# Kernel optimization log

Measured on AMD Instinct MI355X. Metric: run time of the kernel, lower is better.

The kernel has to match this reference:

```python
import jax, jax.numpy as jnp
import numpy as np

S = 1024          # num tokens (single prefill sequence)
H = 2880          # hidden_size
NH = 64           # num query heads
NKV = 8           # num kv heads
HD = 64           # head_dim
G = NH // NKV     # query heads per kv head
THETA = 10000.0
SCALE = HD ** -0.5


def _rope(x, positions):
    # neox-style rotary over full head_dim; x: [S, n_heads, HD]
    half = HD // 2
    inv_freq = 1.0 / (THETA ** (jnp.arange(half, dtype=jnp.float32) / half))
    ang = positions.astype(jnp.float32)[:, None] * inv_freq          # [S, half]
    cos = jnp.cos(ang)[:, None, :]
    sin = jnp.sin(ang)[:, None, :]
    x1, x2 = x[..., :half], x[..., half:]
    return jnp.concatenate([x1 * cos - x2 * sin, x2 * cos + x1 * sin], axis=-1)


def setup_inputs() -> dict:
    key = jax.random.key(0)
    k0, k1, k2, k3 = jax.random.split(key, 4)
    return {
        "positions": jnp.arange(S, dtype=jnp.int32),
        "hidden_states": jax.random.normal(k0, (S, H), dtype=jnp.float32),
        "qkv_w": jax.random.normal(k1, ((NH + 2 * NKV) * HD, H), dtype=jnp.float32) * 0.02,
        "o_w": jax.random.normal(k2, (H, NH * HD), dtype=jnp.float32) * 0.02,
        "sinks": jax.random.normal(k3, (NH,), dtype=jnp.float32),
    }


def reference(positions, hidden_states, qkv_w, o_w, sinks):
    # fused QKV projection (no bias, matching attention_bias=False)
    qkv = hidden_states @ qkv_w.T                                     # [S, 5120]
    q = qkv[:, : NH * HD].reshape(S, NH, HD)
    k = qkv[:, NH * HD : NH * HD + NKV * HD].reshape(S, NKV, HD)
    v = qkv[:, NH * HD + NKV * HD :].reshape(S, NKV, HD)

    # rotary on q and k (rotary_dim == head_dim)
    q = _rope(q, positions)
    k = _rope(k, positions)

    # GQA: group query heads by kv head -> [S, NKV, G, HD]
    qg = q.reshape(S, NKV, G, HD)

    logits = jnp.einsum("qghd,kgd->ghqk", qg, k) * SCALE              # [NKV, G, S, S]
    causal = positions[:, None] >= positions[None, :]                 # [S, S]
    logits = jnp.where(causal[None, None], logits, -jnp.inf)

    # attention sinks: per-head extra logit in the softmax denominator,
    # contributing no value vector.
    sink = sinks.reshape(NKV, G)[:, :, None, None]                    # [NKV, G, 1, 1]
    m = jnp.maximum(jnp.max(logits, axis=-1, keepdims=True), sink)
    p = jnp.exp(logits - m)                                           # [NKV, G, S, S]
    denom = jnp.sum(p, axis=-1, keepdims=True) + jnp.exp(sink - m)
    attn = jnp.einsum("ghqk,kgd->qghd", p / denom, v)                 # [S, NKV, G, HD]

    out = attn.reshape(S, NH * HD) @ o_w.T                            # [S, H]
    return out
```

## Files before the change

### kernel.cpp

```cpp
#include <hip/hip_runtime.h>
#include <hip/hip_bf16.h>
#include <math.h>

#define S_LEN 1024
#define HDIM  2880
#define NH    64
#define NKV   8
#define HD    64
#define QKV_N ((NH + 2*NKV) * HD)
#define O_K   (NH * HD)
#define SCALE 0.125f

typedef _Float16 f16x8 __attribute__((ext_vector_type(8)));
typedef _Float16 f16x4 __attribute__((ext_vector_type(4)));
typedef float    f32x4 __attribute__((ext_vector_type(4)));

__global__ __launch_bounds__(256) void cvt_f32_f16(const float* __restrict__ src,
                                                   _Float16* __restrict__ dst, int n4) {
    const int stride = gridDim.x * blockDim.x;
    for (int i = blockIdx.x * blockDim.x + threadIdx.x; i < n4; i += stride) {
        const float4 v = ((const float4*)src)[i];
        f16x4 p;
        p[0] = (_Float16)v.x; p[1] = (_Float16)v.y;
        p[2] = (_Float16)v.z; p[3] = (_Float16)v.w;
        ((f16x4*)dst)[i] = p;
    }
}

#define CSTR 68
template<typename CT>
__global__ __launch_bounds__(256) void gemm_f16(const _Float16* __restrict__ A,
                                                const float* __restrict__ B,
                                                CT* __restrict__ C,
                                                int M, int N, int K) {
    __shared__ __align__(16) _Float16 sh[16384];

    const int tid  = threadIdx.x;
    const int lane = tid & 63;
    const int wave = tid >> 6;
    const int wr   = wave >> 1;
    const int wc   = wave & 1;
    const int quad = lane >> 4;
    const int fr   = lane & 15;
    const int ks   = quad * 8;
    const int row0 = blockIdx.y * 128;
    const int col0 = blockIdx.x * 128;

    const int klen   = K / (int)gridDim.z;
    const int kb     = (int)blockIdx.z * klen;
    const int nsteps = klen / 32;
    CT* Cp = C + (size_t)blockIdx.z * M * N;

    const int a_cbase0 = wave * 64;
    const int a_ci0 = a_cbase0 + lane;
    const int a_r0 = a_ci0 >> 2, a_ch0 = a_ci0 & 3;
    const int a_cbase1 = 256 + wave * 64;
    const int a_ci1 = a_cbase1 + lane;
    const int a_r1 = a_ci1 >> 2, a_ch1 = a_ci1 & 3;
    int b_r[4], b_ch[4];
#pragma unroll
    for (int it = 0; it < 4; ++it) {
        const int c4 = it * 256 + tid;
        b_r[it]  = c4 >> 3;
        b_ch[it] = (c4 & 7) << 2;
    }

    float4 breg[4];
    f32x4 acc[4][4] = {};

    {
        const _Float16* gp0 = A + (size_t)(row0 + a_r0) * K + kb + a_ch0 * 8;
        __builtin_amdgcn_global_load_lds(
            (const __attribute__((address_space(1))) void*)gp0,
            (__attribute__((address_space(3))) void*)(sh + (size_t)a_cbase0 * 8), 16, 0, 0);
        const _Float16* gp1 = A + (size_t)(row0 + a_r1) * K + kb + a_ch1 * 8;
        __builtin_amdgcn_global_load_lds(
            (const __attribute__((address_space(1))) void*)gp1,
            (__attribute__((address_space(3))) void*)(sh + (size_t)a_cbase1 * 8), 16, 0, 0);
#pragma unroll
        for (int it = 0; it < 4; ++it) {
            int brow = col0 + b_r[it];
            if (brow >= N) brow = N - 1;
            breg[it] = *(const float4*)&B[(size_t)brow * K + kb + b_ch[it]];
        }
        _Float16* Bs0 = sh + 8192;
#pragma unroll
        for (int it = 0; it < 4; ++it) {
            f16x4 p;
            p[0] = (_Float16)breg[it].x; p[1] = (_Float16)breg[it].y;
            p[2] = (_Float16)breg[it].z; p[3] = (_Float16)breg[it].w;
            *(f16x4*)&Bs0[b_r[it] * 32 + b_ch[it]] = p;
        }
    }

    for (int step = 0; step < nsteps; ++step) {
        const int cur = step & 1;
        const int nxt = cur ^ 1;
        _Float16* Acur = sh + cur * 4096;
        _Float16* Anxt = sh + nxt * 4096;
        _Float16* Bcur = sh + 8192 + cur * 4096;
        _Float16* Bnxt = sh + 8192 + nxt * 4096;

        __syncthreads();

        const bool more = (step + 1 < nsteps);
        if (more) {
            const int k1 = kb + (step + 1) * 32;
            const _Float16* gp0 = A + (size_t)(row0 + a_r0) * K + k1 + a_ch0 * 8;
            __builtin_amdgcn_global_load_lds(
                (const __attribute__((address_space(1))) void*)gp0,
                (__attribute__((address_space(3))) void*)(Anxt + (size_t)a_cbase0 * 8), 16, 0, 0);
            const _Float16* gp1 = A + (size_t)(row0 + a_r1) * K + k1 + a_ch1 * 8;
            __builtin_amdgcn_global_load_lds(
                (const __attribute__((address_space(1))) void*)gp1,
                (__attribute__((address_space(3))) void*)(Anxt + (size_t)a_cbase1 * 8), 16, 0, 0);
#pragma unroll
            for (int it = 0; it < 4; ++it) {
                int brow = col0 + b_r[it];
                if (brow >= N) brow = N - 1;
                breg[it] = *(const float4*)&B[(size_t)brow * K + k1 + b_ch[it]];
            }
        }

        f16x8 af[4], bfr[4];
#pragma unroll
        for (int mi = 0; mi < 4; ++mi)
            af[mi] = *(const f16x8*)&Acur[(wr * 64 + mi * 16 + fr) * 32 + ks];
#pragma unroll
        for (int ni = 0; ni < 4; ++ni)
            bfr[ni] = *(const f16x8*)&Bcur[(wc * 64 + ni * 16 + fr) * 32 + ks];
#pragma unroll
        for (int mi = 0; mi < 4; ++mi)
#pragma unroll
            for (int ni = 0; ni < 4; ++ni)
                acc[mi][ni] = __builtin_amdgcn_mfma_f32_16x16x32_f16(
                    af[mi], bfr[ni], acc[mi][ni], 0, 0, 0);

        if (more) {
#pragma unroll
            for (int it = 0; it < 4; ++it) {
                f16x4 p;
                p[0] = (_Float16)breg[it].x; p[1] = (_Float16)breg[it].y;
                p[2] = (_Float16)breg[it].z; p[3] = (_Float16)breg[it].w;
                *(f16x4*)&Bnxt[b_r[it] * 32 + b_ch[it]] = p;
            }
        }
    }

#pragma unroll
    for (int p = 0; p < 2; ++p) {
        __syncthreads();
        if (wc == p) {
#pragma unroll
            for (int mi = 0; mi < 4; ++mi)
#pragma unroll
                for (int ni = 0; ni < 4; ++ni) {
                    const f32x4 v = acc[mi][ni];
#pragma unroll
                    for (int r = 0; r < 4; ++r)
                        sh[(wr * 64 + mi * 16 + quad * 4 + r) * CSTR + ni * 16 + fr] =
                            (_Float16)v[r];
                }
        }
        __syncthreads();
#pragma unroll
        for (int it = 0; it < 4; ++it) {
            const int id  = it * 256 + tid;
            const int row = id >> 3;
            const int ch  = (id & 7) * 8;
            const int col = col0 + p * 64 + ch;
            if (col < N) {
                const f16x4 lo = *(const f16x4*)&sh[row * CSTR + ch];
                const f16x4 hi = *(const f16x4*)&sh[row * CSTR + ch + 4];
                if constexpr (sizeof(CT) == 2) {
                    f16x8 v;
                    v[0]=lo[0]; v[1]=lo[1]; v[2]=lo[2]; v[3]=lo[3];
                    v[4]=hi[0]; v[5]=hi[1]; v[6]=hi[2]; v[7]=hi[3];
                    *(f16x8*)&Cp[(size_t)(row0 + row) * N + col] = v;
                } else {
                    float4 v0 = make_float4((float)lo[0], (float)lo[1],
                                            (float)lo[2], (float)lo[3]);
                    float4 v1 = make_float4((float)hi[0], (float)hi[1],
                                            (float)hi[2], (float)hi[3]);
                    *(float4*)&Cp[(size_t)(row0 + row) * N + col]     = v0;
                    *(float4*)&Cp[(size_t)(row0 + row) * N + col + 4] = v1;
                }
            }
        }
    }
}

__global__ __launch_bounds__(256) void rope_reduce(_Float16* __restrict__ parts,
                                                   int nsplit,
                                                   _Float16* __restrict__ vt,
                                                   const int* __restrict__ positions) {
    __shared__ float buf[QKV_N];
    const int s   = blockIdx.x;
    const int tid = threadIdx.x;
    const size_t PSTR = (size_t)S_LEN * QKV_N;

    for (int c = tid; c < QKV_N / 4; c += 256) {
        float4 a = make_float4(0.f, 0.f, 0.f, 0.f);
        for (int j = 0; j < nsplit; ++j) {
            const f16x4 v = ((const f16x4*)(parts + j * PSTR + (size_t)s * QKV_N))[c];
            a.x += (float)v[0]; a.y += (float)v[1];
            a.z += (float)v[2]; a.w += (float)v[3];
        }
        ((float4*)buf)[c] = a;
    }
    __syncthreads();

    const float pos = (float)positions[s];
    _Float16* orow = parts + (size_t)s * QKV_N;
    for (int w = tid; w < 72 * 32; w += 256) {
        const int h = w >> 5;
        const int t = w & 31;
        const float inv_freq = exp2f(-(float)t * (13.287712379549449f / 32.0f));
        const float ang = pos * inv_freq;
        float sn, cs;
        sincosf(ang, &sn, &cs);
        const float x1 = buf[h * 64 + t];
        const float x2 = buf[h * 64 + t + 32];
        orow[h * 64 + t]      = (_Float16)(x1 * cs - x2 * sn);
        orow[h * 64 + t + 32] = (_Float16)(x2 * cs + x1 * sn);
    }
    for (int c = tid; c < NKV * HD; c += 256)
        vt[(size_t)c * S_LEN + s] = (_Float16)buf[(NH + NKV) * HD + c];
}

__global__ __launch_bounds__(256) void o_reduce(const _Float16* __restrict__ parts,
                                                float* __restrict__ out,
                                                int n4, int nsplit) {
    const size_t PSTR = (size_t)S_LEN * HDIM;
    const int stride = gridDim.x * blockDim.x;
    for (int i = blockIdx.x * blockDim.x + threadIdx.x; i < n4; i += stride) {
        float4 a = make_float4(0.f, 0.f, 0.f, 0.f);
        for (int j = 0; j < nsplit; ++j) {
            const f16x4 v = ((const f16x4*)(parts + j * PSTR))[i];
            a.x += (float)v[0]; a.y += (float)v[1];
            a.z += (float)v[2]; a.w += (float)v[3];
        }
        ((float4*)out)[i] = a;
    }
}

#define LSTR 72
__global__ __launch_bounds__(256) void attn_mfma(const _Float16* __restrict__ qkv,
                                                 const _Float16* __restrict__ vt,
                                                 const float* __restrict__ sinks,
                                                 const int* __restrict__ positions,
                                                 _Float16* __restrict__ attn_out) {
    __shared__ __align__(16) _Float16 Ks[2][64 * LSTR];
    __shared__ __align__(16) _Float16 Vs[2][64 * LSTR];
    __shared__ __align__(16) _Float16 Ps[64 * LSTR];

    const int tid  = threadIdx.x;
    const int lane = tid & 63;
    const int wave = tid >> 6;
    const int fr   = lane & 15;
    const int quad = lane >> 4;
    const int ks8  = quad * 8;
    const int n    = blockIdx.x;
    const int qt   = (int)gridDim.y - 1 - (int)blockIdx.y;
    const int g    = n >> 3;

    int st_r[2], st_o[2];
#pragma unroll
    for (int it = 0; it < 2; ++it) {
        const int c = it * 256 + tid;
        st_r[it] = c >> 3;
        st_o[it] = (c & 7) * 8;
    }

    const _Float16* qrow = qkv + (size_t)(qt * 64 + wave * 16 + fr) * QKV_N + n * HD;
    const f16x8 a_q0 = *(const f16x8*)&qrow[ks8];
    const f16x8 a_q1 = *(const f16x8*)&qrow[32 + ks8];

    int pq[4];
#pragma unroll
    for (int r = 0; r < 4; ++r)
        pq[r] = positions[qt * 64 + wave * 16 + quad * 4 + r];

    const float sinkv = sinks[n];
    float m[4], l[4];
    f32x4 o[4] = {};
#pragma unroll
    for (int r = 0; r < 4; ++r) { m[r] = sinkv; l[r] = 1.0f; }

    f16x8 kreg[2], vreg[2];
    {
        const _Float16* Kg = qkv + (size_t)0 * QKV_N + NH * HD + g * HD;
        const _Float16* Vg = vt + (size_t)(g * HD) * S_LEN;
#pragma unroll
        for (int it = 0; it < 2; ++it) {
            kreg[it] = *(const f16x8*)&Kg[(size_t)st_r[it] * QKV_N + st_o[it]];
            vreg[it] = *(const f16x8*)&Vg[(size_t)st_r[it] * S_LEN + st_o[it]];
        }
#pragma unroll
        for (int it = 0; it < 2; ++it) {
            *(f16x8*)&Ks[0][st_r[it] * LSTR + st_o[it]] = kreg[it];
            *(f16x8*)&Vs[0][st_r[it] * LSTR + st_o[it]] = vreg[it];
        }
    }

    for (int kt = 0; kt <= qt; ++kt) {
        const int cur = kt & 1;
        const int nxt = cur ^ 1;
        __syncthreads();

        const bool more = (kt < qt);
        if (more) {
            const _Float16* Kg = qkv + (size_t)((kt + 1) * 64) * QKV_N + NH * HD + g * HD;
            const _Float16* Vg = vt + (size_t)(g * HD) * S_LEN + (kt + 1) * 64;
#pragma unroll
            for (int it = 0; it < 2; ++it) {
                kreg[it] = *(const f16x8*)&Kg[(size_t)st_r[it] * QKV_N + st_o[it]];
                vreg[it] = *(const f16x8*)&Vg[(size_t)st_r[it] * S_LEN + st_o[it]];
            }
        }

        f32x4 s[4] = {};
#pragma unroll
        for (int nt = 0; nt < 4; ++nt) {
            const f16x8 b0 = *(const f16x8*)&Ks[cur][(nt * 16 + fr) * LSTR + ks8];
            s[nt] = __builtin_amdgcn_mfma_f32_16x16x32_f16(a_q0, b0, s[nt], 0, 0, 0);
            const f16x8 b1 = *(const f16x8*)&Ks[cur][(nt * 16 + fr) * LSTR + 32 + ks8];
            s[nt] = __builtin_amdgcn_mfma_f32_16x16x32_f16(a_q1, b1, s[nt], 0, 0, 0);
        }

        const bool diag = (kt == qt);
        int pk[4];
        if (diag) {
#pragma unroll
            for (int nt = 0; nt < 4; ++nt) pk[nt] = positions[qt * 64 + nt * 16 + fr];
        }
#pragma unroll
        for (int nt = 0; nt < 4; ++nt)
#pragma unroll
            for (int r = 0; r < 4; ++r) {
                float sv = s[nt][r] * SCALE;
                if (diag && pk[nt] > pq[r]) sv = -3.0e38f;
                s[nt][r] = sv;
            }

#pragma unroll
        for (int r = 0; r < 4; ++r) {
            float tm = fmaxf(fmaxf(s[0][r], s[1][r]), fmaxf(s[2][r], s[3][r]));
            tm = fmaxf(tm, __shfl_xor(tm, 1, 64));
            tm = fmaxf(tm, __shfl_xor(tm, 2, 64));
            tm = fmaxf(tm, __shfl_xor(tm, 4, 64));
            tm = fmaxf(tm, __shfl_xor(tm, 8, 64));
            const float nm = fmaxf(m[r], tm);
            const float alpha = __expf(m[r] - nm);
            float rs = 0.0f;
#pragma unroll
            for (int nt = 0; nt < 4; ++nt) {
                const float p = __expf(s[nt][r] - nm);
                s[nt][r] = p;
                rs += p;
            }
            rs += __shfl_xor(rs, 1, 64);
            rs += __shfl_xor(rs, 2, 64);
            rs += __shfl_xor(rs, 4, 64);
            rs += __shfl_xor(rs, 8, 64);
            l[r] = l[r] * alpha + rs;
            m[r] = nm;
#pragma unroll
            for (int nt = 0; nt < 4; ++nt) o[nt][r] *= alpha;
        }

#pragma unroll
        for (int nt = 0; nt < 4; ++nt)
#pragma unroll
            for (int r = 0; r < 4; ++r)
                Ps[(wave * 16 + quad * 4 + r) * LSTR + nt * 16 + fr] = (_Float16)s[nt][r];
        __threadfence_block();

#pragma unroll
        for (int k2 = 0; k2 < 2; ++k2) {
            const f16x8 ap = *(const f16x8*)&Ps[(wave * 16 + fr) * LSTR + k2 * 32 + ks8];
#pragma unroll
            for (int nt = 0; nt < 4; ++nt) {
                const f16x8 bv = *(const f16x8*)&Vs[cur][(nt * 16 + fr) * LSTR + k2 * 32 + ks8];
                o[nt] = __builtin_amdgcn_mfma_f32_16x16x32_f16(ap, bv, o[nt], 0, 0, 0);
            }
        }

        if (more) {
#pragma unroll
            for (int it = 0; it < 2; ++it) {
                *(f16x8*)&Ks[nxt][st_r[it] * LSTR + st_o[it]] = kreg[it];
                *(f16x8*)&Vs[nxt][st_r[it] * LSTR + st_o[it]] = vreg[it];
            }
        }
    }

#pragma unroll
    for (int r = 0; r < 4; ++r) {
        const float inv = 1.0f / l[r];
        const size_t row = (size_t)(qt * 64 + wave * 16 + quad * 4 + r);
#pragma unroll
        for (int nt = 0; nt < 4; ++nt)
            attn_out[row * O_K + n * HD + nt * 16 + fr] = (_Float16)(o[nt][r] * inv);
    }
}

extern "C" void kernel_launch(void* const* d_in, const int* in_sizes, int n_in,
                              void* d_out, int out_size, void* d_ws, size_t ws_size,
                              hipStream_t stream) {
    const int*   positions = (const int*)d_in[0];
    const float* hidden    = (const float*)d_in[1];
    const float* qkv_w     = (const float*)d_in[2];
    const float* o_w       = (const float*)d_in[3];
    const float* sinks     = (const float*)d_in[4];
    float* out = (float*)d_out;

    const size_t n_hid  = (size_t)S_LEN * HDIM;
    const size_t n_qkv  = (size_t)S_LEN * QKV_N;
    const size_t n_attn = (size_t)S_LEN * O_K;
    const size_t n_vt   = (size_t)NKV * HD * S_LEN;
    const size_t n_out  = (size_t)S_LEN * HDIM;

    const int SP_Q = 3;
    const int SP_O = 4;

    const size_t need = (n_hid + SP_Q * n_qkv + n_attn + n_vt) * sizeof(_Float16);

    if (ws_size >= need) {
        _Float16* hid_h  = (_Float16*)d_ws;
        _Float16* qkvp   = hid_h + n_hid;
        _Float16* attn_h = qkvp + SP_Q * n_qkv;
        _Float16* vt     = attn_h + n_attn;
        _Float16* opart  = qkvp;

        cvt_f32_f16<<<512, 256, 0, stream>>>(hidden, hid_h, (int)(n_hid / 4));
        gemm_f16<_Float16><<<dim3(QKV_N / 128, S_LEN / 128, SP_Q), 256, 0, stream>>>(
            hid_h, qkv_w, qkvp, S_LEN, QKV_N, HDIM);
        rope_reduce<<<S_LEN, 256, 0, stream>>>(qkvp, SP_Q, vt, positions);
        attn_mfma<<<dim3(NH, S_LEN / 64), 256, 0, stream>>>(qkvp, vt, sinks, positions, attn_h);
        gemm_f16<_Float16><<<dim3((HDIM + 127) / 128, S_LEN / 128, SP_O), 256, 0, stream>>>(
            attn_h, o_w, opart, S_LEN, HDIM, O_K);
        o_reduce<<<1024, 256, 0, stream>>>(opart, out, (int)(n_out / 4), SP_O);
    } else {
        _Float16* hid_h  = (_Float16*)d_ws;
        _Float16* qkvp   = hid_h + n_hid;
        _Float16* attn_h = qkvp + n_qkv;
        _Float16* vt     = attn_h + n_attn;

        cvt_f32_f16<<<512, 256, 0, stream>>>(hidden, hid_h, (int)(n_hid / 4));
        gemm_f16<_Float16><<<dim3(QKV_N / 128, S_LEN / 128, 1), 256, 0, stream>>>(
            hid_h, qkv_w, qkvp, S_LEN, QKV_N, HDIM);
        rope_reduce<<<S_LEN, 256, 0, stream>>>(qkvp, 1, vt, positions);
        attn_mfma<<<dim3(NH, S_LEN / 64), 256, 0, stream>>>(qkvp, vt, sinks, positions, attn_h);
        gemm_f16<float><<<dim3((HDIM + 127) / 128, S_LEN / 128, 1), 256, 0, stream>>>(
            attn_h, o_w, out, S_LEN, HDIM, O_K);
    }
}
```

Measured before the change: 304.7 us.

## Pre-convert weights to fp16 and load both GEMM operands via direct LDS DMA

Adds a single conversion kernel that casts hidden states, QKV weights and output weights to fp16 in workspace. A new GEMM variant then loads both A and B tiles with global_load_lds DMA instead of register-staged fp32 loads followed by in-kernel conversion. The aim is to halve the GEMM's weight read traffic and drop the conversion and LDS store work from the inner loop. In exchange, every call pays an extra full read and fp16 write of both weight matrices, and it needs more workspace, with the old path kept as a fallback.

```diff
diff --git a/kernel.cpp b/kernel.cpp
--- a/kernel.cpp
+++ b/kernel.cpp
@@ -15,24 +15,46 @@
 typedef _Float16 f16x4 __attribute__((ext_vector_type(4)));
 typedef float    f32x4 __attribute__((ext_vector_type(4)));
 
+__device__ __forceinline__ void cvt4(const float* __restrict__ s,
+                                     _Float16* __restrict__ d, int i) {
+    const float4 v = ((const float4*)s)[i];
+    f16x4 p;
+    p[0] = (_Float16)v.x; p[1] = (_Float16)v.y;
+    p[2] = (_Float16)v.z; p[3] = (_Float16)v.w;
+    ((f16x4*)d)[i] = p;
+}
+
 __global__ __launch_bounds__(256) void cvt_f32_f16(const float* __restrict__ src,
                                                    _Float16* __restrict__ dst, int n4) {
     const int stride = gridDim.x * blockDim.x;
-    for (int i = blockIdx.x * blockDim.x + threadIdx.x; i < n4; i += stride) {
-        const float4 v = ((const float4*)src)[i];
-        f16x4 p;
-        p[0] = (_Float16)v.x; p[1] = (_Float16)v.y;
-        p[2] = (_Float16)v.z; p[3] = (_Float16)v.w;
-        ((f16x4*)dst)[i] = p;
-    }
+    for (int i = blockIdx.x * blockDim.x + threadIdx.x; i < n4; i += stride)
+        cvt4(src, dst, i);
+}
+
+__global__ __launch_bounds__(256) void cvt_all(const float* __restrict__ h,
+                                               const float* __restrict__ qw,
+                                               const float* __restrict__ ow,
+                                               _Float16* __restrict__ dh,
+                                               _Float16* __restrict__ dqw,
+                                               _Float16* __restrict__ dow) {
+    const int stride = gridDim.x * blockDim.x;
+    const int t0 = blockIdx.x * blockDim.x + threadIdx.x;
+    for (int i = t0; i < 737280;  i += stride) cvt4(h,  dh,  i);
+    for (int i = t0; i < 3686400; i += stride) cvt4(qw, dqw, i);
+    for (int i = t0; i < 2949120; i += stride) cvt4(ow, dow, i);
 }
 
 #define CSTR 68
+
+#define DMA16(GP, LP) __builtin_amdgcn_global_load_lds( \
+        (const __attribute__((address_space(1))) void*)(GP), \
+        (__attribute__((address_space(3))) void*)(LP), 16, 0, 0)
+
 template<typename CT>
-__global__ __launch_bounds__(256) void gemm_f16(const _Float16* __restrict__ A,
-                                                const float* __restrict__ B,
-                                                CT* __restrict__ C,
-                                                int M, int N, int K) {
+__global__ __launch_bounds__(256) void gemm_ff(const _Float16* __restrict__ A,
+                                               const _Float16* __restrict__ B,
+                                               CT* __restrict__ C,
+                                               int M, int N, int K) {
     __shared__ __align__(16) _Float16 sh[16384];
 
     const int tid  = threadIdx.x;
@@ -51,100 +73,57 @@
     const int nsteps = klen / 32;
     CT* Cp = C + (size_t)blockIdx.z * M * N;
 
-    const int a_cbase0 = wave * 64;
-    const int a_ci0 = a_cbase0 + lane;
-    const int a_r0 = a_ci0 >> 2, a_ch0 = a_ci0 & 3;
-    const int a_cbase1 = 256 + wave * 64;
-    const int a_ci1 = a_cbase1 + lane;
-    const int a_r1 = a_ci1 >> 2, a_ch1 = a_ci1 & 3;
-    int b_r[4], b_ch[4];
-#pragma unroll
-    for (int it = 0; it < 4; ++it) {
-        const int c4 = it * 256 + tid;
-        b_r[it]  = c4 >> 3;
-        b_ch[it] = (c4 & 7) << 2;
-    }
-
-    float4 breg[4];
+    const int r0   = tid >> 2;
+    const int ch   = (tid & 3) * 8;
+    const int dst0 = (tid & ~63) * 8;
+
+    const size_t aoff0 = (size_t)(row0 + r0)      * K;
+    const size_t aoff1 = (size_t)(row0 + r0 + 64) * K;
+    int bR0 = col0 + r0;      if (bR0 >= N) bR0 = N - 1;
+    int bR1 = col0 + r0 + 64; if (bR1 >= N) bR1 = N - 1;
+    const size_t boff0 = (size_t)bR0 * K;
+    const size_t boff1 = (size_t)bR1 * K;
+
     f32x4 acc[4][4] = {};
 
     {
-        const _Float16* gp0 = A + (size_t)(row0 + a_r0) * K + kb + a_ch0 * 8;
-        __builtin_amdgcn_global_load_lds(
-            (const __attribute__((address_space(1))) void*)gp0,
-            (__attribute__((address_space(3))) void*)(sh + (size_t)a_cbase0 * 8), 16, 0, 0);
-        const _Float16* gp1 = A + (size_t)(row0 + a_r1) * K + kb + a_ch1 * 8;
-        __builtin_amdgcn_global_load_lds(
-            (const __attribute__((address_space(1))) void*)gp1,
-            (__attribute__((address_space(3))) void*)(sh + (size_t)a_cbase1 * 8), 16, 0, 0);
-#pragma unroll
-        for (int it = 0; it < 4; ++it) {
-            int brow = col0 + b_r[it];
-            if (brow >= N) brow = N - 1;
-            breg[it] = *(const float4*)&B[(size_t)brow * K + kb + b_ch[it]];
-        }
-        _Float16* Bs0 = sh + 8192;
-#pragma unroll
-        for (int it = 0; it < 4; ++it) {
-            f16x4 p;
-            p[0] = (_Float16)breg[it].x; p[1] = (_Float16)breg[it].y;
-            p[2] = (_Float16)breg[it].z; p[3] = (_Float16)breg[it].w;
-            *(f16x4*)&Bs0[b_r[it] * 32 + b_ch[it]] = p;
-        }
+        const int kk = kb + ch;
+        DMA16(A + aoff0 + kk, sh + dst0);
+        DMA16(A + aoff1 + kk, sh + 2048 + dst0);
+        DMA16(B + boff0 + kk, sh + 8192 + dst0);
+        DMA16(B + boff1 + kk, sh + 8192 + 2048 + dst0);
     }
 
     for (int step = 0; step < nsteps; ++step) {
         const int cur = step & 1;
-        const int nxt = cur ^ 1;
         _Float16* Acur = sh + cur * 4096;
-        _Float16* Anxt = sh + nxt * 4096;
+        _Float16* Anxt = sh + (cur ^ 1) * 4096;
         _Float16* Bcur = sh + 8192 + cur * 4096;
-        _Float16* Bnxt = sh + 8192 + nxt * 4096;
+        _Float16* Bnxt = sh + 8192 + (cur ^ 1) * 4096;
 
         __syncthreads();
 
-        const bool more = (step + 1 < nsteps);
-        if (more) {
-            const int k1 = kb + (step + 1) * 32;
-            const _Float16* gp0 = A + (size_t)(row0 + a_r0) * K + k1 + a_ch0 * 8;
-            __builtin_amdgcn_global_load_lds(
-                (const __attribute__((address_space(1))) void*)gp0,
-                (__attribute__((address_space(3))) void*)(Anxt + (size_t)a_cbase0 * 8), 16, 0, 0);
-            const _Float16* gp1 = A + (size_t)(row0 + a_r1) * K + k1 + a_ch1 * 8;
-            __builtin_amdgcn_global_load_lds(
-                (const __attribute__((address_space(1))) void*)gp1,
-                (__attribute__((address_space(3))) void*)(Anxt + (size_t)a_cbase1 * 8), 16, 0, 0);
-#pragma unroll
-            for (int it = 0; it < 4; ++it) {
-                int brow = col0 + b_r[it];
-                if (brow >= N) brow = N - 1;
-                breg[it] = *(const float4*)&B[(size_t)brow * K + k1 + b_ch[it]];
-            }
-        }
-
-        f16x8 af[4], bfr[4];
+        if (step + 1 < nsteps) {
+            const int k1 = kb + (step + 1) * 32 + ch;
+            DMA16(A + aoff0 + k1, Anxt + dst0);
+            DMA16(A + aoff1 + k1, Anxt + 2048 + dst0);
+            DMA16(B + boff0 + k1, Bnxt + dst0);
+            DMA16(B + boff1 + k1, Bnxt + 2048 + dst0);
+        }
+
+        f16x8 af[4], bf[4];
 #pragma unroll
         for (int mi = 0; mi < 4; ++mi)
             af[mi] = *(const f16x8*)&Acur[(wr * 64 + mi * 16 + fr) * 32 + ks];
 #pragma unroll
         for (int ni = 0; ni < 4; ++ni)
-            bfr[ni] = *(const f16x8*)&Bcur[(wc * 64 + ni * 16 + fr) * 32 + ks];
+            bf[ni] = *(const f16x8*)&Bcur[(wc * 64 + ni * 16 + fr) * 32 + ks];
 #pragma unroll
         for (int mi = 0; mi < 4; ++mi)
 #pragma unroll
             for (int ni = 0; ni < 4; ++ni)
                 acc[mi][ni] = __builtin_amdgcn_mfma_f32_16x16x32_f16(
-                    af[mi], bfr[ni], acc[mi][ni], 0, 0, 0);
-
-        if (more) {
-#pragma unroll
-            for (int it = 0; it < 4; ++it) {
-                f16x4 p;
-                p[0] = (_Float16)breg[it].x; p[1] = (_Float16)breg[it].y;
-                p[2] = (_Float16)breg[it].z; p[3] = (_Float16)breg[it].w;
-                *(f16x4*)&Bnxt[b_r[it] * 32 + b_ch[it]] = p;
-            }
-        }
+                    af[mi], bf[ni], acc[mi][ni], 0, 0, 0);
     }
 
 #pragma unroll
@@ -167,11 +146,11 @@
         for (int it = 0; it < 4; ++it) {
             const int id  = it * 256 + tid;
             const int row = id >> 3;
-            const int ch  = (id & 7) * 8;
-            const int col = col0 + p * 64 + ch;
+            const int chh = (id & 7) * 8;
+            const int col = col0 + p * 64 + chh;
             if (col < N) {
-                const f16x4 lo = *(const f16x4*)&sh[row * CSTR + ch];
-                const f16x4 hi = *(const f16x4*)&sh[row * CSTR + ch + 4];
+                const f16x4 lo = *(const f16x4*)&sh[row * CSTR + chh];
+                const f16x4 hi = *(const f16x4*)&sh[row * CSTR + chh + 4];
                 if constexpr (sizeof(CT) == 2) {
                     f16x8 v;
                     v[0]=lo[0]; v[1]=lo[1]; v[2]=lo[2]; v[3]=lo[3];
@@ -190,6 +169,160 @@
     }
 }
 
+template<typename CT>
+__global__ __launch_bounds__(256) void gemm_f16(const _Float16* __restrict__ A,
+                                                const float* __restrict__ B,
+                                                CT* __restrict__ C,
+                                                int M, int N, int K) {
+    __shared__ __align__(16) _Float16 sh[16384];
+
+    const int tid  = threadIdx.x;
+    const int lane = tid & 63;
+    const int wave = tid >> 6;
+    const int wr   = wave >> 1;
+    const int wc   = wave & 1;
+    const int quad = lane >> 4;
+    const int fr   = lane & 15;
+    const int ks   = quad * 8;
+    const int row0 = blockIdx.y * 128;
+    const int col0 = blockIdx.x * 128;
+
+    const int klen   = K / (int)gridDim.z;
+    const int kb     = (int)blockIdx.z * klen;
+    const int nsteps = klen / 32;
+    CT* Cp = C + (size_t)blockIdx.z * M * N;
+
+    const int a_cbase0 = wave * 64;
+    const int a_ci0 = a_cbase0 + lane;
+    const int a_r0 = a_ci0 >> 2, a_ch0 = a_ci0 & 3;
+    const int a_cbase1 = 256 + wave * 64;
+    const int a_ci1 = a_cbase1 + lane;
+    const int a_r1 = a_ci1 >> 2, a_ch1 = a_ci1 & 3;
+    int b_r[4], b_ch[4];
+#pragma unroll
+    for (int it = 0; it < 4; ++it) {
+        const int c4 = it * 256 + tid;
+        b_r[it]  = c4 >> 3;
+        b_ch[it] = (c4 & 7) << 2;
+    }
+
+    float4 breg[4];
+    f32x4 acc[4][4] = {};
+
+    {
+        const _Float16* gp0 = A + (size_t)(row0 + a_r0) * K + kb + a_ch0 * 8;
+        DMA16(gp0, sh + (size_t)a_cbase0 * 8);
+        const _Float16* gp1 = A + (size_t)(row0 + a_r1) * K + kb + a_ch1 * 8;
+        DMA16(gp1, sh + (size_t)a_cbase1 * 8);
+#pragma unroll
+        for (int it = 0; it < 4; ++it) {
+            int brow = col0 + b_r[it];
+            if (brow >= N) brow = N - 1;
+            breg[it] = *(const float4*)&B[(size_t)brow * K + kb + b_ch[it]];
+        }
+        _Float16* Bs0 = sh + 8192;
+#pragma unroll
+        for (int it = 0; it < 4; ++it) {
+            f16x4 p;
+            p[0] = (_Float16)breg[it].x; p[1] = (_Float16)breg[it].y;
+            p[2] = (_Float16)breg[it].z; p[3] = (_Float16)breg[it].w;
+            *(f16x4*)&Bs0[b_r[it] * 32 + b_ch[it]] = p;
+        }
+    }
+
+    for (int step = 0; step < nsteps; ++step) {
+        const int cur = step & 1;
+        const int nxt = cur ^ 1;
+        _Float16* Acur = sh + cur * 4096;
+        _Float16* Anxt = sh + nxt * 4096;
+        _Float16* Bcur = sh + 8192 + cur * 4096;
+        _Float16* Bnxt = sh + 8192 + nxt * 4096;
+
+        __syncthreads();
+
+        const bool more = (step + 1 < nsteps);
+        if (more) {
+            const int k1 = kb + (step + 1) * 32;
+            const _Float16* gp0 = A + (size_t)(row0 + a_r0) * K + k1 + a_ch0 * 8;
+            DMA16(gp0, Anxt + (size_t)a_cbase0 * 8);
+            const _Float16* gp1 = A + (size_t)(row0 + a_r1) * K + k1 + a_ch1 * 8;
+            DMA16(gp1, Anxt + (size_t)a_cbase1 * 8);
+#pragma unroll
+            for (int it = 0; it < 4; ++it) {
+                int brow = col0 + b_r[it];
+                if (brow >= N) brow = N - 1;
+                breg[it] = *(const float4*)&B[(size_t)brow * K + k1 + b_ch[it]];
+            }
+        }
+
+        f16x8 af[4], bfr[4];
+#pragma unroll
+        for (int mi = 0; mi < 4; ++mi)
+            af[mi] = *(const f16x8*)&Acur[(wr * 64 + mi * 16 + fr) * 32 + ks];
+#pragma unroll
+        for (int ni = 0; ni < 4; ++ni)
+            bfr[ni] = *(const f16x8*)&Bcur[(wc * 64 + ni * 16 + fr) * 32 + ks];
+#pragma unroll
+        for (int mi = 0; mi < 4; ++mi)
+#pragma unroll
+            for (int ni = 0; ni < 4; ++ni)
+                acc[mi][ni] = __builtin_amdgcn_mfma_f32_16x16x32_f16(
+                    af[mi], bfr[ni], acc[mi][ni], 0, 0, 0);
+
+        if (more) {
+#pragma unroll
+            for (int it = 0; it < 4; ++it) {
+                f16x4 p;
+                p[0] = (_Float16)breg[it].x; p[1] = (_Float16)breg[it].y;
+                p[2] = (_Float16)breg[it].z; p[3] = (_Float16)breg[it].w;
+                *(f16x4*)&Bnxt[b_r[it] * 32 + b_ch[it]] = p;
+            }
+        }
+    }
+
+#pragma unroll
+    for (int p = 0; p < 2; ++p) {
+        __syncthreads();
+        if (wc == p) {
+#pragma unroll
+            for (int mi = 0; mi < 4; ++mi)
+#pragma unroll
+                for (int ni = 0; ni < 4; ++ni) {
+                    const f32x4 v = acc[mi][ni];
+#pragma unroll
+                    for (int r = 0; r < 4; ++r)
+                        sh[(wr * 64 + mi * 16 + quad * 4 + r) * CSTR + ni * 16 + fr] =
+                            (_Float16)v[r];
+                }
+        }
+        __syncthreads();
+#pragma unroll
+        for (int it = 0; it < 4; ++it) {
+            const int id  = it * 256 + tid;
+            const int row = id >> 3;
+            const int chh = (id & 7) * 8;
+            const int col = col0 + p * 64 + chh;
+            if (col < N) {
+                const f16x4 lo = *(const f16x4*)&sh[row * CSTR + chh];
+                const f16x4 hi = *(const f16x4*)&sh[row * CSTR + chh + 4];
+                if constexpr (sizeof(CT) == 2) {
+                    f16x8 v;
+                    v[0]=lo[0]; v[1]=lo[1]; v[2]=lo[2]; v[3]=lo[3];
+                    v[4]=hi[0]; v[5]=hi[1]; v[6]=hi[2]; v[7]=hi[3];
+                    *(f16x8*)&Cp[(size_t)(row0 + row) * N + col] = v;
+                } else {
+                    float4 v0 = make_float4((float)lo[0], (float)lo[1],
+                                            (float)lo[2], (float)lo[3]);
+                    float4 v1 = make_float4((float)hi[0], (float)hi[1],
+                                            (float)hi[2], (float)hi[3]);
+                    *(float4*)&Cp[(size_t)(row0 + row) * N + col]     = v0;
+                    *(float4*)&Cp[(size_t)(row0 + row) * N + col + 4] = v1;
+                }
+            }
+        }
+    }
+}
+
 __global__ __launch_bounds__(256) void rope_reduce(_Float16* __restrict__ parts,
                                                    int nsplit,
                                                    _Float16* __restrict__ vt,
@@ -420,13 +553,34 @@
     const size_t n_attn = (size_t)S_LEN * O_K;
     const size_t n_vt   = (size_t)NKV * HD * S_LEN;
     const size_t n_out  = (size_t)S_LEN * HDIM;
+    const size_t n_qw   = (size_t)QKV_N * HDIM;
+    const size_t n_ow   = (size_t)HDIM * O_K;
 
     const int SP_Q = 3;
     const int SP_O = 4;
 
-    const size_t need = (n_hid + SP_Q * n_qkv + n_attn + n_vt) * sizeof(_Float16);
-
-    if (ws_size >= need) {
+    const size_t need_full =
+        (n_hid + SP_Q * n_qkv + n_attn + n_vt + n_qw + n_ow) * sizeof(_Float16);
+    const size_t need_mid  = (n_hid + SP_Q * n_qkv + n_attn + n_vt) * sizeof(_Float16);
+
+    if (ws_size >= need_full) {
+        _Float16* hid_h  = (_Float16*)d_ws;
+        _Float16* qkvp   = hid_h + n_hid;
+        _Float16* attn_h = qkvp + SP_Q * n_qkv;
+        _Float16* vt     = attn_h + n_attn;
+        _Float16* qw_h   = vt + n_vt;
+        _Float16* ow_h   = qw_h + n_qw;
+        _Float16* opart  = qkvp;
+
+        cvt_all<<<2048, 256, 0, stream>>>(hidden, qkv_w, o_w, hid_h, qw_h, ow_h);
+        gemm_ff<_Float16><<<dim3(QKV_N / 128, S_LEN / 128, SP_Q), 256, 0, stream>>>(
+            hid_h, qw_h, qkvp, S_LEN, QKV_N, HDIM);
+        rope_reduce<<<S_LEN, 256, 0, stream>>>(qkvp, SP_Q, vt, positions);
+        attn_mfma<<<dim3(NH, S_LEN / 64), 256, 0, stream>>>(qkvp, vt, sinks, positions, attn_h);
+        gemm_ff<_Float16><<<dim3((HDIM + 127) / 128, S_LEN / 128, SP_O), 256, 0, stream>>>(
+            attn_h, ow_h, opart, S_LEN, HDIM, O_K);
+        o_reduce<<<1024, 256, 0, stream>>>(opart, out, (int)(n_out / 4), SP_O);
+    } else if (ws_size >= need_mid) {
         _Float16* hid_h  = (_Float16*)d_ws;
         _Float16* qkvp   = hid_h + n_hid;
         _Float16* attn_h = qkvp + SP_Q * n_qkv;
```

Measured after the change: 298.4 us. -2.1%, faster.
